# Performance work log

Measured on AMD Instinct MI355X. Metric: run time of the kernel, lower is better.

The kernel has to match this reference:

```python
import jax, jax.numpy as jnp
import numpy as np

PAD_VALUE = 0.0


def setup_inputs() -> dict:
    key = jax.random.key(0)
    k1, k2 = jax.random.split(key)
    B, T, D = 32, 512, 384
    xs = jax.random.normal(k1, (B, T, D), dtype=jnp.float32)
    ds = jax.random.randint(k2, (B, T), 0, 8, dtype=jnp.int32)
    return {"xs": xs, "ds": ds, "max_frame": 4096}


def reference(xs, ds, max_frame):
    """LengthRegulator forward (alpha == 1.0).

    xs: (B, T, D) float token embeddings
    ds: (B, T) int durations (zero-duration tokens are skipped)
    max_frame: python int; output is padded/stacked to (B, max_frame, D)
    """
    B, T, D = xs.shape
    cum = jnp.cumsum(ds, axis=1)                      # (B, T) exclusive-end offsets
    total = cum[:, -1]                                # (B,) total frames per sequence
    t = jnp.arange(max_frame, dtype=cum.dtype)        # (F,)
    # token index producing frame t: first i with cum[i] > t (skips d==0 tokens)
    idx = jax.vmap(lambda c: jnp.searchsorted(c, t, side="right"))(cum)  # (B, F)
    idx = jnp.minimum(idx, T - 1)
    out = jnp.take_along_axis(xs, idx[:, :, None], axis=1)               # (B, F, D)
    valid = (t[None, :] < total[:, None])[:, :, None]                    # (B, F, 1)
    return jnp.where(valid, out, jnp.asarray(PAD_VALUE, xs.dtype))
```

## Files before the change

### kernel.cpp

```cpp
#include <hip/hip_runtime.h>
#include <hip/hip_bf16.h>

constexpr int B  = 32;
constexpr int T  = 512;
constexpr int D  = 384;
constexpr int MF = 4096;
constexpr int D4 = D / 4;

__global__ __launch_bounds__(T) void lr_build_map(const int* __restrict__ ds,
                                                  int* __restrict__ map) {
    const int b = blockIdx.x;
    const int i = threadIdx.x;

    __shared__ int s[T];
    const int d = ds[b * T + i];
    s[i] = d;
    __syncthreads();

    #pragma unroll
    for (int off = 1; off < T; off <<= 1) {
        int v = (i >= off) ? s[i - off] : 0;
        __syncthreads();
        s[i] += v;
        __syncthreads();
    }

    const int incl  = s[i];
    const int excl  = incl - d;
    const int total = s[T - 1];

    int* m = map + b * MF;

    for (int t = min(total, MF) + i; t < MF; t += T) m[t] = -1;

    const int end = min(incl, MF);
    for (int t = excl; t < end; ++t) m[t] = i;
}

__global__ __launch_bounds__(256) void lr_gather(const float4* __restrict__ xs4,
                                                 const int* __restrict__ map,
                                                 float4* __restrict__ out4,
                                                 int n4) {
    int g = blockIdx.x * blockDim.x + threadIdx.x;
    const int stride = gridDim.x * blockDim.x;
    for (; g < n4; g += stride) {
        const int row = g / D4;
        const int q   = g - row * D4;
        const int b   = row / MF;
        const int idx = map[row];
        float4 v;
        if (idx >= 0) {
            v = xs4[(b * T + idx) * D4 + q];
        } else {
            v = make_float4(0.f, 0.f, 0.f, 0.f);
        }
        out4[g] = v;
    }
}

extern "C" void kernel_launch(void* const* d_in, const int* in_sizes, int n_in,
                              void* d_out, int out_size, void* d_ws, size_t ws_size,
                              hipStream_t stream) {
    const float* xs = (const float*)d_in[0];
    const int*   ds = (const int*)d_in[1];

    float* out = (float*)d_out;
    int*   map = (int*)d_ws;

    lr_build_map<<<B, T, 0, stream>>>(ds, map);

    const int n4 = out_size / 4;
    const int block = 256;
    const int grid = 4096;
    lr_gather<<<grid, block, 0, stream>>>((const float4*)xs, map,
                                          (float4*)out, n4);
}
```

Measured before the change: 43.09 us.

## Fuse map building and gather into one kernel with per-chunk binary search

Replaces the two-kernel scheme (scan plus scatter map to workspace, then grid-stride gather) with a single kernel where each block recomputes the prefix sum of durations for its batch in shared memory. It then binary-searches token indices for a 256-frame chunk and gathers rows with nontemporal stores. This removes one launch, the global map round trip and the serialized scatter loop over long durations. In exchange every block redundantly recomputes the 512-element scan.

```diff
diff --git a/kernel.cpp b/kernel.cpp
--- a/kernel.cpp
+++ b/kernel.cpp
@@ -1,60 +1,66 @@
 #include <hip/hip_runtime.h>
 #include <hip/hip_bf16.h>
 
-constexpr int B  = 32;
-constexpr int T  = 512;
-constexpr int D  = 384;
-constexpr int MF = 4096;
-constexpr int D4 = D / 4;
+constexpr int B     = 32;
+constexpr int T     = 512;
+constexpr int D     = 384;
+constexpr int MF    = 4096;
+constexpr int D4    = D / 4;
+constexpr int CHUNK = 256;
+constexpr int BLOCK = 512;
+constexpr int ITERS = CHUNK * D4 / BLOCK;
 
-__global__ __launch_bounds__(T) void lr_build_map(const int* __restrict__ ds,
-                                                  int* __restrict__ map) {
-    const int b = blockIdx.x;
-    const int i = threadIdx.x;
+typedef float f32x4 __attribute__((ext_vector_type(4)));
 
-    __shared__ int s[T];
-    const int d = ds[b * T + i];
-    s[i] = d;
+__global__ __launch_bounds__(BLOCK) void lr_fused(const float* __restrict__ xs,
+                                                  const int* __restrict__ ds,
+                                                  float* __restrict__ out) {
+    const int b    = blockIdx.y;
+    const int base = blockIdx.x * CHUNK;
+    const int tid  = threadIdx.x;
+
+    __shared__ int cum[T];
+    __shared__ int map_l[CHUNK];
+
+    cum[tid] = ds[b * T + tid];
+    __syncthreads();
+    #pragma unroll
+    for (int off = 1; off < T; off <<= 1) {
+        int v = (tid >= off) ? cum[tid - off] : 0;
+        __syncthreads();
+        cum[tid] += v;
+        __syncthreads();
+    }
+    const int total = cum[T - 1];
+
+    if (tid < CHUNK) {
+        const int f = base + tid;
+        int m = -1;
+        if (f < total) {
+            int lo = 0, hi = T;
+            while (lo < hi) {
+                const int mid = (lo + hi) >> 1;
+                if (cum[mid] <= f) lo = mid + 1; else hi = mid;
+            }
+            m = lo;
+        }
+        map_l[tid] = m;
+    }
     __syncthreads();
 
-    #pragma unroll
-    for (int off = 1; off < T; off <<= 1) {
-        int v = (i >= off) ? s[i - off] : 0;
-        __syncthreads();
-        s[i] += v;
-        __syncthreads();
-    }
+    const f32x4* __restrict__ xs4 = (const f32x4*)(xs) + (size_t)b * T * D4;
+    f32x4* __restrict__ out4 = (f32x4*)(out) + ((size_t)b * MF + base) * D4;
 
-    const int incl  = s[i];
-    const int excl  = incl - d;
-    const int total = s[T - 1];
-
-    int* m = map + b * MF;
-
-    for (int t = min(total, MF) + i; t < MF; t += T) m[t] = -1;
-
-    const int end = min(incl, MF);
-    for (int t = excl; t < end; ++t) m[t] = i;
-}
-
-__global__ __launch_bounds__(256) void lr_gather(const float4* __restrict__ xs4,
-                                                 const int* __restrict__ map,
-                                                 float4* __restrict__ out4,
-                                                 int n4) {
-    int g = blockIdx.x * blockDim.x + threadIdx.x;
-    const int stride = gridDim.x * blockDim.x;
-    for (; g < n4; g += stride) {
-        const int row = g / D4;
-        const int q   = g - row * D4;
-        const int b   = row / MF;
-        const int idx = map[row];
-        float4 v;
-        if (idx >= 0) {
-            v = xs4[(b * T + idx) * D4 + q];
-        } else {
-            v = make_float4(0.f, 0.f, 0.f, 0.f);
-        }
-        out4[g] = v;
+    int f = tid / D4;
+    int q = tid - f * D4;
+    #pragma unroll 4
+    for (int it = 0; it < ITERS; ++it) {
+        const int tok = map_l[f];
+        f32x4 v = {0.f, 0.f, 0.f, 0.f};
+        if (tok >= 0) v = xs4[tok * D4 + q];
+        __builtin_nontemporal_store(v, &out4[f * D4 + q]);
+        f += 5; q += 32;
+        if (q >= D4) { q -= D4; ++f; }
     }
 }
 
@@ -65,13 +71,7 @@
     const int*   ds = (const int*)d_in[1];
 
     float* out = (float*)d_out;
-    int*   map = (int*)d_ws;
 
-    lr_build_map<<<B, T, 0, stream>>>(ds, map);
-
-    const int n4 = out_size / 4;
-    const int block = 256;
-    const int grid = 4096;
-    lr_gather<<<grid, block, 0, stream>>>((const float4*)xs, map,
-                                          (float4*)out, n4);
+    dim3 grid(MF / CHUNK, B);
+    lr_fused<<<grid, BLOCK, 0, stream>>>(xs, ds, out);
 }
```

After: 46.77 us. 8.6% more time.
